# Kernel tuning notes

Measured on AMD Instinct MI355X. Metric: run time of the kernel, lower is better.

The kernel has to match this reference:

```python
import jax, jax.numpy as jnp
import numpy as np

L, B, N, D, H, F = 6, 4, 1024, 1024, 16, 4096
HD = D // H
EPS = 1e-5


def setup_inputs() -> dict:
    key = jax.random.key(0)
    ks = jax.random.split(key, 20)
    s = 0.02
    inp = {
        "feats": jax.random.normal(ks[0], (L, B, N, D), jnp.float32),
        "enc_out": jax.random.normal(ks[1], (B, N, D), jnp.float32),
        "trg_mask": jnp.zeros((1, 1, N, N), jnp.float32),
        "src_mask": jnp.zeros((1, 1, N, N), jnp.float32),
    }
    # stacked per-layer parameters, torch Linear convention W:[out,in]
    names = ["wq1", "wk1", "wv1", "wo1", "wq2", "wk2", "wv2", "wo2"]
    for i, n in enumerate(names):
        inp[n] = jax.random.normal(ks[2 + i], (L, D, D), jnp.float32) * s
        inp["b" + n[1:]] = jnp.zeros((L, D), jnp.float32)
    inp["wf1"] = jax.random.normal(ks[10], (L, F, D), jnp.float32) * s
    inp["bf1"] = jnp.zeros((L, F), jnp.float32)
    inp["wf2"] = jax.random.normal(ks[11], (L, D, F), jnp.float32) * s
    inp["bf2"] = jnp.zeros((L, D), jnp.float32)
    for j in (1, 2, 3):
        inp[f"g{j}"] = jnp.ones((L, D), jnp.float32)
        inp[f"be{j}"] = jnp.zeros((L, D), jnp.float32)
    return inp


def _ln(x, g, b):
    m = jnp.mean(x, -1, keepdims=True)
    v = jnp.mean(jnp.square(x - m), -1, keepdims=True)
    return (x - m) * jax.lax.rsqrt(v + EPS) * g + b


def _heads(x):  # [B,N,D] -> [B,H,N,HD]
    return x.reshape(x.shape[0], x.shape[1], H, HD).transpose(0, 2, 1, 3)


def _mha(q_in, k_in, v_in, Wq, bq, Wk, bk, Wv, bv, Wo, bo, mask):
    q = _heads(q_in @ Wq.T + bq) * (HD ** -0.5)
    k = _heads(k_in @ Wk.T + bk)
    v = _heads(v_in @ Wv.T + bv)
    attn = jnp.einsum("bhid,bhjd->bhij", q, k) + mask
    attn = jax.nn.softmax(attn, axis=-1)
    o = jnp.einsum("bhij,bhjd->bhid", attn, v)
    o = o.transpose(0, 2, 1, 3).reshape(q_in.shape[0], q_in.shape[1], D)
    return o @ Wo.T + bo


def reference(feats, enc_out, trg_mask, src_mask,
              wq1, bq1, wk1, bk1, wv1, bv1, wo1, bo1,
              wq2, bq2, wk2, bk2, wv2, bv2, wo2, bo2,
              wf1, bf1, wf2, bf2, g1, be1, g2, be2, g3, be3):
    x = enc_out
    outs = []
    for l in range(L):
        feat = feats[l]
        dec_out = x
        # cross-attn to encoder output (attn1, src_mask)
        y = _mha(feat, enc_out, enc_out,
                 wq1[l], bq1[l], wk1[l], bk1[l], wv1[l], bv1[l], wo1[l], bo1[l],
                 src_mask) + feat
        y = _ln(y, g1[l], be1[l])
        # attn to previous decoder output (attn2, trg_mask)
        y = _mha(y, dec_out, dec_out,
                 wq2[l], bq2[l], wk2[l], bk2[l], wv2[l], bv2[l], wo2[l], bo2[l],
                 trg_mask) + y
        y = _ln(y, g2[l], be2[l])
        # FFN
        h = jax.nn.relu(y @ wf1[l].T + bf1[l])
        y = _ln(h @ wf2[l].T + bf2[l] + y, g3[l], be3[l])
        outs.append(y)
        x = y
    return jnp.stack(outs)  # [L,B,N,D]
```

## Files before the change

### kernel.cpp

```cpp
#include <hip/hip_runtime.h>
#include <cstdint>
#include <cstddef>

#define Lc 6
#define Bc 4
#define Nc 1024
#define Dc 1024
#define Hn 16
#define HDc 64
#define Fc 4096

static constexpr long BND = (long)Bc * Nc * Dc;
static constexpr long DD  = (long)Dc * Dc;
#define FDl  ((long)Fc * Dc)
static constexpr long BNF = (long)Bc * Nc * Fc;

typedef __attribute__((ext_vector_type(8))) short bf8_t;
typedef __attribute__((ext_vector_type(4))) float f4_t;

__device__ __forceinline__ float b2f(unsigned short u) {
  union { unsigned int i; float f; } v; v.i = ((unsigned int)u) << 16; return v.f;
}
__device__ __forceinline__ unsigned short f2b(float f) {
  union { float f; unsigned int i; } v; v.f = f;
  return (unsigned short)((v.i + 0x7fffu + ((v.i >> 16) & 1u)) >> 16);
}

__device__ __forceinline__ void gl_lds16(const unsigned short* g, unsigned short* l) {
  __builtin_amdgcn_global_load_lds(
      (const __attribute__((address_space(1))) void*)g,
      (__attribute__((address_space(3))) void*)l, 16, 0, 0);
}

__global__ __launch_bounds__(256) void k_cast(const float* __restrict__ x,
                                              unsigned short* __restrict__ y, long n4) {
  long i = (long)blockIdx.x * 256 + threadIdx.x;
  if (i >= n4) return;
  float4 v = ((const float4*)x)[i];
  ushort4 o = { f2b(v.x), f2b(v.y), f2b(v.z), f2b(v.w) };
  ((ushort4*)y)[i] = o;
}

__global__ __launch_bounds__(256) void k_cast2(const float* __restrict__ s1,
                                               const float* __restrict__ s2,
                                               unsigned short* __restrict__ dst) {
  long i4 = (long)blockIdx.x * 256 + threadIdx.x;
  long flat = i4 * 4;
  int l = (int)(flat / (2 * DD));
  long r = flat - (long)l * 2 * DD;
  const float* src = (r < DD) ? (s1 + (long)l * DD + r) : (s2 + (long)l * DD + (r - DD));
  float4 v = *(const float4*)src;
  ushort4 o = { f2b(v.x), f2b(v.y), f2b(v.z), f2b(v.w) };
  *(ushort4*)(dst + flat) = o;
}

__global__ __launch_bounds__(256) void k_bcat2(const float* __restrict__ b1,
                                               const float* __restrict__ b2,
                                               float* __restrict__ dst) {
  int i = blockIdx.x * 256 + threadIdx.x;
  int l = i >> 11, r = i & 2047;
  dst[i] = (r < 1024) ? b1[l * 1024 + r] : b2[l * 1024 + (r - 1024)];
}

__global__ __launch_bounds__(256) void k_packvt2(const unsigned short* __restrict__ KV,
                                                 unsigned short* __restrict__ Vt) {
  __shared__ unsigned short T[64][72];
  const int bh = blockIdx.y, b = bh >> 4, h = bh & 15;
  const int n0 = blockIdx.x * 64;
  const int r = threadIdx.x >> 4;
  const int c4 = (threadIdx.x & 15) * 4;
  const unsigned short* src = KV + ((long)b * Nc + n0) * 2048 + 1024 + h * 64;
  #pragma unroll
  for (int it = 0; it < 4; ++it) {
    ushort4 v = *(const ushort4*)&src[(long)(it * 16 + r) * 2048 + c4];
    *(ushort4*)&T[it * 16 + r][c4] = v;
  }
  __syncthreads();
  unsigned short* dst = Vt + (long)bh * HDc * Nc + n0;
  #pragma unroll
  for (int it = 0; it < 4; ++it) {
    const int d = it * 16 + r;
    ushort4 v = { T[c4 + 0][d], T[c4 + 1][d], T[c4 + 2][d], T[c4 + 3][d] };
    *(ushort4*)&dst[(long)d * Nc + c4] = v;
  }
}

__global__ __launch_bounds__(256) void k_ln(const float* __restrict__ X,
                                            const float* __restrict__ X2,
                                            const float* __restrict__ g,
                                            const float* __restrict__ be,
                                            float* __restrict__ Yf,
                                            unsigned short* __restrict__ Yb) {
  const long row = blockIdx.x;
  const float4* x4 = (const float4*)(X + row * Dc);
  const int tid = threadIdx.x, lane = tid & 63, wave = tid >> 6;
  float4 x = x4[tid];
  if (X2) {
    float4 x2 = ((const float4*)(X2 + row * Dc))[tid];
    x.x += x2.x; x.y += x2.y; x.z += x2.z; x.w += x2.w;
  }
  float s = x.x + x.y + x.z + x.w;
  float q = x.x * x.x + x.y * x.y + x.z * x.z + x.w * x.w;
  #pragma unroll
  for (int o = 32; o > 0; o >>= 1) { s += __shfl_down(s, o); q += __shfl_down(q, o); }
  __shared__ float rs[4], rq[4];
  if (lane == 0) { rs[wave] = s; rq[wave] = q; }
  __syncthreads();
  s = rs[0] + rs[1] + rs[2] + rs[3];
  q = rq[0] + rq[1] + rq[2] + rq[3];
  const float mean = s * (1.f / Dc);
  const float var = q * (1.f / Dc) - mean * mean;
  const float rstd = rsqrtf(var + 1e-5f);
  float4 gv = ((const float4*)g)[tid];
  float4 bv = ((const float4*)be)[tid];
  float4 y;
  y.x = (x.x - mean) * rstd * gv.x + bv.x;
  y.y = (x.y - mean) * rstd * gv.y + bv.y;
  y.z = (x.z - mean) * rstd * gv.z + bv.z;
  y.w = (x.w - mean) * rstd * gv.w + bv.w;
  if (Yf) ((float4*)(Yf + row * Dc))[tid] = y;
  if (Yb) {
    ushort4 o = { f2b(y.x), f2b(y.y), f2b(y.z), f2b(y.w) };
    ((ushort4*)(Yb + row * Dc))[tid] = o;
  }
}

#define QT 64
#define KT 128
#define PRS 132
__global__ __launch_bounds__(256, 2) void k_flash(
    const unsigned short* __restrict__ Q,
    const unsigned short* __restrict__ Kg,
    const unsigned short* __restrict__ Vt,
    const float* __restrict__ mask,
    unsigned short* __restrict__ O, int ldk) {
  __shared__ __align__(16) unsigned short Qs[QT * 64];
  __shared__ __align__(16) unsigned short Ks[KT * 64];
  __shared__ __align__(16) unsigned short Vs[64 * KT];
  __shared__ __align__(16) unsigned short Ps[QT * PRS];

  const int tid = threadIdx.x;
  const int wave = tid >> 6, lane = tid & 63;
  const int lm = lane & 15, quad = lane >> 4;
  const int bh = blockIdx.y;
  const int b = bh >> 4, h = bh & 15;
  const int q0 = blockIdx.x * QT;

  const unsigned short* Qb = Q + ((long)b * Nc + q0) * Dc + h * HDc;
  const unsigned short* Kb = Kg + (long)b * Nc * ldk + h * HDc;
  const unsigned short* Vb = Vt + (long)bh * HDc * Nc;

  const int sr = tid >> 3, sc = (tid & 7) * 8;
  #pragma unroll
  for (int it = 0; it < QT / 32; ++it)
    gl_lds16(Qb + (long)(it * 32 + sr) * Dc + sc, &Qs[(it * 32 + sr) * 64 + sc]);

  f4_t Oa[4];
  #pragma unroll
  for (int jh = 0; jh < 4; ++jh) Oa[jh] = {0.f, 0.f, 0.f, 0.f};
  float m_run[4], l_run[4];
  #pragma unroll
  for (int r = 0; r < 4; ++r) { m_run[r] = -1e30f; l_run[r] = 0.f; }

  const int row_q = wave * 16 + quad * 4;
  const int vr = tid >> 4, vc = (tid & 15) * 8;

  for (int t = 0; t < Nc / KT; ++t) {
    #pragma unroll
    for (int it = 0; it < KT / 32; ++it)
      gl_lds16(Kb + (long)(t * KT + it * 32 + sr) * ldk + sc, &Ks[(it * 32 + sr) * 64 + sc]);
    #pragma unroll
    for (int it = 0; it < 4; ++it)
      gl_lds16(Vb + (long)(it * 16 + vr) * Nc + t * KT + vc, &Vs[(it * 16 + vr) * KT + vc]);
    __syncthreads();

    f4_t Sa[8];
    #pragma unroll
    for (int j = 0; j < 8; ++j) Sa[j] = {0.f, 0.f, 0.f, 0.f};
    #pragma unroll
    for (int kk = 0; kk < 2; ++kk) {
      const int kq = kk * 32 + quad * 8;
      bf8_t aq = *(const bf8_t*)&Qs[(wave * 16 + lm) * 64 + kq];
      #pragma unroll
      for (int j = 0; j < 8; ++j) {
        bf8_t bk = *(const bf8_t*)&Ks[(j * 16 + lm) * 64 + kq];
        Sa[j] = __builtin_amdgcn_mfma_f32_16x16x32_bf16(aq, bk, Sa[j], 0, 0, 0);
      }
    }

    float p[8][4], alpha[4];
    #pragma unroll
    for (int r = 0; r < 4; ++r) {
      const float* mrow = mask + (long)(q0 + row_q + r) * Nc + t * KT + lm;
      float sv[8];
      float mt = -1e30f;
      #pragma unroll
      for (int j = 0; j < 8; ++j) { sv[j] = Sa[j][r] + mrow[j * 16]; mt = fmaxf(mt, sv[j]); }
      #pragma unroll
      for (int o = 1; o < 16; o <<= 1) mt = fmaxf(mt, __shfl_xor(mt, o));
      const float mn = fmaxf(m_run[r], mt);
      alpha[r] = __expf(m_run[r] - mn);
      m_run[r] = mn;
      float sp = 0.f;
      #pragma unroll
      for (int j = 0; j < 8; ++j) { float e = __expf(sv[j] - mn); p[j][r] = e; sp += e; }
      #pragma unroll
      for (int o = 1; o < 16; o <<= 1) sp += __shfl_xor(sp, o);
      l_run[r] = l_run[r] * alpha[r] + sp;
    }

    #pragma unroll
    for (int r = 0; r < 4; ++r)
      #pragma unroll
      for (int j = 0; j < 8; ++j)
        Ps[(row_q + r) * PRS + j * 16 + lm] = f2b(p[j][r]);
    __syncthreads();

    #pragma unroll
    for (int jh = 0; jh < 4; ++jh)
      #pragma unroll
      for (int r = 0; r < 4; ++r) Oa[jh][r] *= alpha[r];
    #pragma unroll
    for (int kk = 0; kk < 4; ++kk) {
      const int kp = kk * 32 + quad * 8;
      bf8_t ap = *(const bf8_t*)&Ps[(wave * 16 + lm) * PRS + kp];
      #pragma unroll
      for (int jh = 0; jh < 4; ++jh) {
        bf8_t bv = *(const bf8_t*)&Vs[(jh * 16 + lm) * KT + kp];
        Oa[jh] = __builtin_amdgcn_mfma_f32_16x16x32_bf16(ap, bv, Oa[jh], 0, 0, 0);
      }
    }
    __syncthreads();
  }

  #pragma unroll
  for (int r = 0; r < 4; ++r) {
    const float inv = 1.f / l_run[r];
    unsigned short* orow = O + ((long)b * Nc + q0 + row_q + r) * Dc + h * HDc;
    #pragma unroll
    for (int jh = 0; jh < 4; ++jh) orow[jh * 16 + lm] = f2b(Oa[jh][r] * inv);
  }
}

template <int BM, int BN, int MW, int NW>
__device__ __forceinline__ void mfma_loop(
    const unsigned short* __restrict__ A, const unsigned short* __restrict__ W,
    int K, int lda, int ldb, int m0, int n0,
    unsigned short* As, unsigned short* Bs,
    f4_t (&acc)[BM / MW / 16][BN / NW / 16]) {
  constexpr int WM = BM / MW, WN = BN / NW;
  constexpr int FM = WM / 16, FN = WN / 16;
  const int tid = threadIdx.x;
  const int wave = tid >> 6, lane = tid & 63;
  const int wm = wave / NW, wn = wave % NW;
  const int sr = tid >> 3, sc = (tid & 7) * 8;
  const int lm = lane & 15, quad = lane >> 4;

  for (int k0 = 0; k0 < K; k0 += 64) {
    #pragma unroll
    for (int it = 0; it < BM / 32; ++it) {
      const int rr = it * 32 + sr;
      gl_lds16(A + (long)(m0 + rr) * lda + (k0 + sc), &As[rr * 64 + sc]);
    }
    #pragma unroll
    for (int it = 0; it < BN / 32; ++it) {
      const int rr = it * 32 + sr;
      gl_lds16(W + (long)(n0 + rr) * ldb + (k0 + sc), &Bs[rr * 64 + sc]);
    }
    __syncthreads();
    #pragma unroll
    for (int kk = 0; kk < 2; ++kk) {
      const int kq = kk * 32 + quad * 8;
      bf8_t af[FM], bfr[FN];
      #pragma unroll
      for (int i = 0; i < FM; ++i)
        af[i] = *(const bf8_t*)&As[(wm * WM + i * 16 + lm) * 64 + kq];
      #pragma unroll
      for (int j = 0; j < FN; ++j)
        bfr[j] = *(const bf8_t*)&Bs[(wn * WN + j * 16 + lm) * 64 + kq];
      #pragma unroll
      for (int i = 0; i < FM; ++i)
        #pragma unroll
        for (int j = 0; j < FN; ++j)
          acc[i][j] = __builtin_amdgcn_mfma_f32_16x16x32_bf16(af[i], bfr[j], acc[i][j], 0, 0, 0);
    }
    __syncthreads();
  }
}

template <int BM, int BN, int MW, int NW>
__global__ __launch_bounds__(256, 2) void gemm_bt(
    const unsigned short* __restrict__ A, const unsigned short* __restrict__ W,
    const float* __restrict__ bias, const float* __restrict__ res,
    float* __restrict__ Cf, unsigned short* __restrict__ Cb,
    int K, int lda, int ldb, int ldc, float scale, int relu) {
  constexpr int WM = BM / MW, WN = BN / NW;
  constexpr int FM = WM / 16, FN = WN / 16;

  __shared__ __align__(16) unsigned short As[BM * 64];
  __shared__ __align__(16) unsigned short Bs[BN * 64];

  const int tid = threadIdx.x;
  const int wave = tid >> 6, lane = tid & 63;
  const int wm = wave / NW, wn = wave % NW;
  const int n0 = blockIdx.x * BN, m0 = blockIdx.y * BM;
  const int lm = lane & 15, quad = lane >> 4;

  f4_t acc[FM][FN];
  const f4_t zero = {0.f, 0.f, 0.f, 0.f};
  #pragma unroll
  for (int i = 0; i < FM; ++i)
    #pragma unroll
    for (int j = 0; j < FN; ++j) acc[i][j] = zero;

  mfma_loop<BM, BN, MW, NW>(A, W, K, lda, ldb, m0, n0, As, Bs, acc);

  #pragma unroll
  for (int i = 0; i < FM; ++i) {
    const int grow_base = m0 + wm * WM + i * 16 + quad * 4;
    #pragma unroll
    for (int j = 0; j < FN; ++j) {
      const int gcol = n0 + wn * WN + j * 16 + lm;
      const float bi = bias ? bias[gcol] : 0.f;
      #pragma unroll
      for (int r = 0; r < 4; ++r) {
        float v = (acc[i][j][r] + bi) * scale;
        if (relu) v = fmaxf(v, 0.f);
        const long cidx = (long)(grow_base + r) * ldc + gcol;
        if (res) v += res[cidx];
        if (Cf) Cf[cidx] = v;
        if (Cb) Cb[cidx] = f2b(v);
      }
    }
  }
}

__global__ __launch_bounds__(256, 2) void gemm_qkv(
    const unsigned short* __restrict__ Aq,  const unsigned short* __restrict__ Wq,
    const float* __restrict__ bq,
    const unsigned short* __restrict__ Ak1, const unsigned short* __restrict__ Wkv1,
    const float* __restrict__ bkv1,
    const unsigned short* __restrict__ Ak2, const unsigned short* __restrict__ Wkv2,
    const float* __restrict__ bkv2,
    unsigned short* __restrict__ Cq, unsigned short* __restrict__ Ckv1,
    unsigned short* __restrict__ Ckv2) {
  __shared__ __align__(16) unsigned short As[128 * 64];
  __shared__ __align__(16) unsigned short Bs[128 * 64];

  const int bx = blockIdx.x;
  const unsigned short *A, *W;
  const float* bias;
  unsigned short* C;
  int ldc, n0;
  float scale;
  if (bx < 8)       { A = Aq;  W = Wq;   bias = bq;   C = Cq;   ldc = 1024; n0 = bx * 128;        scale = 0.125f; }
  else if (bx < 24) { A = Ak1; W = Wkv1; bias = bkv1; C = Ckv1; ldc = 2048; n0 = (bx - 8) * 128;  scale = 1.f; }
  else              { A = Ak2; W = Wkv2; bias = bkv2; C = Ckv2; ldc = 2048; n0 = (bx - 24) * 128; scale = 1.f; }
  const int m0 = blockIdx.y * 128;

  const int tid = threadIdx.x;
  const int wave = tid >> 6, lane = tid & 63;
  const int wm = wave / 2, wn = wave % 2;
  const int lm = lane & 15, quad = lane >> 4;

  f4_t acc[4][4];
  const f4_t zero = {0.f, 0.f, 0.f, 0.f};
  #pragma unroll
  for (int i = 0; i < 4; ++i)
    #pragma unroll
    for (int j = 0; j < 4; ++j) acc[i][j] = zero;

  mfma_loop<128, 128, 2, 2>(A, W, 1024, 1024, 1024, m0, n0, As, Bs, acc);

  #pragma unroll
  for (int i = 0; i < 4; ++i) {
    const int grow_base = m0 + wm * 64 + i * 16 + quad * 4;
    #pragma unroll
    for (int j = 0; j < 4; ++j) {
      const int gcol = n0 + wn * 64 + j * 16 + lm;
      const float bi = bias[gcol];
      #pragma unroll
      for (int r = 0; r < 4; ++r) {
        float v = (acc[i][j][r] + bi) * scale;
        C[(long)(grow_base + r) * ldc + gcol] = f2b(v);
      }
    }
  }
}

__global__ __launch_bounds__(256, 2) void gemm_f2s(
    const unsigned short* __restrict__ A, const unsigned short* __restrict__ W,
    const float* __restrict__ bias, const float* __restrict__ res,
    float* __restrict__ P0, float* __restrict__ P1) {
  __shared__ __align__(16) unsigned short As[128 * 64];
  __shared__ __align__(16) unsigned short Bs[128 * 64];

  const int z = blockIdx.z;
  const int kbeg = z * 2048;
  const int n0 = blockIdx.x * 128, m0 = blockIdx.y * 128;

  const int tid = threadIdx.x;
  const int wave = tid >> 6, lane = tid & 63;
  const int wm = wave / 2, wn = wave % 2;
  const int lm = lane & 15, quad = lane >> 4;

  f4_t acc[4][4];
  const f4_t zero = {0.f, 0.f, 0.f, 0.f};
  #pragma unroll
  for (int i = 0; i < 4; ++i)
    #pragma unroll
    for (int j = 0; j < 4; ++j) acc[i][j] = zero;

  mfma_loop<128, 128, 2, 2>(A + kbeg, W + kbeg, 2048, 4096, 4096, m0, n0, As, Bs, acc);

  float* P = z ? P1 : P0;
  #pragma unroll
  for (int i = 0; i < 4; ++i) {
    const int grow_base = m0 + wm * 64 + i * 16 + quad * 4;
    #pragma unroll
    for (int j = 0; j < 4; ++j) {
      const int gcol = n0 + wn * 64 + j * 16 + lm;
      const float bi = bias[gcol];
      #pragma unroll
      for (int r = 0; r < 4; ++r) {
        const long cidx = (long)(grow_base + r) * Dc + gcol;
        float v = acc[i][j][r];
        if (z == 0) v += bi + res[cidx];
        P[cidx] = v;
      }
    }
  }
}

extern "C" void kernel_launch(void* const* d_in, const int* in_sizes, int n_in,
                              void* d_out, int out_size, void* d_ws, size_t ws_size,
                              hipStream_t stream) {
  const float* feats    = (const float*)d_in[0];
  const float* enc      = (const float*)d_in[1];
  const float* trg_mask = (const float*)d_in[2];
  const float* src_mask = (const float*)d_in[3];
  const float* wq1 = (const float*)d_in[4];  const float* bq1 = (const float*)d_in[5];
  const float* wk1 = (const float*)d_in[6];  const float* bk1 = (const float*)d_in[7];
  const float* wv1 = (const float*)d_in[8];  const float* bv1 = (const float*)d_in[9];
  const float* wo1 = (const float*)d_in[10]; const float* bo1 = (const float*)d_in[11];
  const float* wq2 = (const float*)d_in[12]; const float* bq2 = (const float*)d_in[13];
  const float* wk2 = (const float*)d_in[14]; const float* bk2 = (const float*)d_in[15];
  const float* wv2 = (const float*)d_in[16]; const float* bv2 = (const float*)d_in[17];
  const float* wo2 = (const float*)d_in[18]; const float* bo2 = (const float*)d_in[19];
  const float* wf1 = (const float*)d_in[20]; const float* bf1 = (const float*)d_in[21];
  const float* wf2 = (const float*)d_in[22]; const float* bf2 = (const float*)d_in[23];
  const float* g1  = (const float*)d_in[24]; const float* be1 = (const float*)d_in[25];
  const float* g2  = (const float*)d_in[26]; const float* be2 = (const float*)d_in[27];
  const float* g3  = (const float*)d_in[28]; const float* be3 = (const float*)d_in[29];
  float* out = (float*)d_out;

  char* wsp = (char*)d_ws;
  size_t off = 0;
  auto alloc = [&](size_t bytes) -> void* {
    void* p = wsp + off;
    off = (off + bytes + 255) & ~(size_t)255;
    return p;
  };
  unsigned short* wq1b  = (unsigned short*)alloc(Lc * DD * 2);
  unsigned short* wo1b  = (unsigned short*)alloc(Lc * DD * 2);
  unsigned short* wq2b  = (unsigned short*)alloc(Lc * DD * 2);
  unsigned short* wo2b  = (unsigned short*)alloc(Lc * DD * 2);
  unsigned short* wkv1b = (unsigned short*)alloc(Lc * 2 * DD * 2);
  unsigned short* wkv2b = (unsigned short*)alloc(Lc * 2 * DD * 2);
  unsigned short* wf1b  = (unsigned short*)alloc(Lc * FDl * 2);
  unsigned short* wf2b  = (unsigned short*)alloc(Lc * FDl * 2);
  float* bkv1c = (float*)alloc(Lc * 2048 * 4);
  float* bkv2c = (float*)alloc(Lc * 2048 * 4);
  unsigned short* encb    = (unsigned short*)alloc(BND * 2);
  unsigned short* featall = (unsigned short*)alloc(Lc * BND * 2);
  unsigned short* xb    = (unsigned short*)alloc(BND * 2);
  unsigned short* y1b   = (unsigned short*)alloc(BND * 2);
  unsigned short* y2b   = (unsigned short*)alloc(BND * 2);
  unsigned short* qb    = (unsigned short*)alloc(BND * 2);
  unsigned short* kvb   = (unsigned short*)alloc((long)Bc * Nc * 2048 * 2);
  unsigned short* kvb2  = (unsigned short*)alloc((long)Bc * Nc * 2048 * 2);
  unsigned short* vtb   = (unsigned short*)alloc(BND * 2);
  unsigned short* vtb2  = (unsigned short*)alloc(BND * 2);
  unsigned short* ob    = (unsigned short*)alloc(BND * 2);
  unsigned short* hb    = (unsigned short*)alloc(BNF * 2);
  float* y1f  = (float*)alloc(BND * 4);
  float* y2f  = (float*)alloc(BND * 4);
  float* pre  = (float*)alloc(BND * 4);
  float* pre2 = (float*)alloc(BND * 4);
  (void)ws_size; (void)in_sizes; (void)n_in; (void)out_size;

  auto cast = [&](const float* src, unsigned short* dst, long n) {
    long n4 = n / 4;
    k_cast<<<dim3((unsigned)((n4 + 255) / 256)), dim3(256), 0, stream>>>(src, dst, n4);
  };
  auto cast2 = [&](const float* s1, const float* s2, unsigned short* dst) {
    k_cast2<<<dim3((unsigned)(Lc * 2 * DD / 4 / 256)), dim3(256), 0, stream>>>(s1, s2, dst);
  };
  auto bcat2 = [&](const float* b1, const float* b2, float* dst) {
    k_bcat2<<<dim3(Lc * 2048 / 256), dim3(256), 0, stream>>>(b1, b2, dst);
  };
  auto gemm128 = [&](const unsigned short* A, const unsigned short* Wp, const float* bias,
                     const float* res, float* Cf, unsigned short* Cb,
                     int M, int Nout, int K, int lda, int ldb, int ldc, float scale, int relu) {
    gemm_bt<128, 128, 2, 2><<<dim3(Nout / 128, M / 128), dim3(256), 0, stream>>>(
        A, Wp, bias, res, Cf, Cb, K, lda, ldb, ldc, scale, relu);
  };
  auto gemm64 = [&](const unsigned short* A, const unsigned short* Wp, const float* bias,
                    const float* res, float* Cf, unsigned short* Cb,
                    int M, int Nout, int K, int lda, int ldb, int ldc, float scale, int relu) {
    gemm_bt<128, 64, 2, 2><<<dim3(Nout / 64, M / 128), dim3(256), 0, stream>>>(
        A, Wp, bias, res, Cf, Cb, K, lda, ldb, ldc, scale, relu);
  };
  auto flash = [&](const unsigned short* Kg, const unsigned short* Vt, const float* mask) {
    k_flash<<<dim3(Nc / QT, Bc * Hn), dim3(256), 0, stream>>>(qb, Kg, Vt, mask, ob, 2048);
  };
  auto ln = [&](const float* X, const float* X2, const float* gg, const float* bb,
                float* Yf, unsigned short* Yb) {
    k_ln<<<dim3(Bc * Nc), dim3(256), 0, stream>>>(X, X2, gg, bb, Yf, Yb);
  };
  auto packvt = [&](const unsigned short* kv, unsigned short* vt) {
    k_packvt2<<<dim3(Nc / 64, Bc * Hn), dim3(256), 0, stream>>>(kv, vt);
  };

  cast(wq1, wq1b, Lc * DD); cast(wo1, wo1b, Lc * DD);
  cast(wq2, wq2b, Lc * DD); cast(wo2, wo2b, Lc * DD);
  cast2(wk1, wv1, wkv1b);   cast2(wk2, wv2, wkv2b);
  bcat2(bk1, bv1, bkv1c);   bcat2(bk2, bv2, bkv2c);
  cast(wf1, wf1b, Lc * FDl); cast(wf2, wf2b, Lc * FDl);
  cast(enc, encb, BND);
  cast(feats, featall, (long)Lc * BND);

  for (int l = 0; l < Lc; ++l) {
    const float* featl = feats + (long)l * BND;
    const unsigned short* featb = featall + (long)l * BND;
    const unsigned short* kv2src = (l == 0) ? encb : xb;

    gemm_qkv<<<dim3(40, 32), dim3(256), 0, stream>>>(
        featb, wq1b + (long)l * DD, bq1 + l * Dc,
        encb,  wkv1b + (long)l * 2 * DD, bkv1c + l * 2048,
        kv2src, wkv2b + (long)l * 2 * DD, bkv2c + l * 2048,
        qb, kvb, kvb2);
    packvt(kvb, vtb);
    packvt(kvb2, vtb2);

    flash(kvb, vtb, src_mask);
    gemm64(ob, wo1b + (long)l * DD, bo1 + l * Dc, featl, pre, nullptr,
           Bc * Nc, Dc, Dc, Dc, Dc, Dc, 1.f, 0);
    ln(pre, nullptr, g1 + l * Dc, be1 + l * Dc, y1f, y1b);

    gemm64(y1b, wq2b + (long)l * DD, bq2 + l * Dc, nullptr, nullptr, qb,
           Bc * Nc, Dc, Dc, Dc, Dc, Dc, 0.125f, 0);
    flash(kvb2, vtb2, trg_mask);
    gemm64(ob, wo2b + (long)l * DD, bo2 + l * Dc, y1f, pre, nullptr,
           Bc * Nc, Dc, Dc, Dc, Dc, Dc, 1.f, 0);
    ln(pre, nullptr, g2 + l * Dc, be2 + l * Dc, y2f, y2b);

    gemm128(y2b, wf1b + (long)l * FDl, bf1 + l * Fc, nullptr, nullptr, hb,
            Bc * Nc, Fc, Dc, Dc, Dc, Fc, 1.f, 1);
    gemm_f2s<<<dim3(8, 32, 2), dim3(256), 0, stream>>>(
        hb, wf2b + (long)l * FDl, bf2 + l * Dc, y2f, pre, pre2);
    ln(pre, pre2, g3 + l * Dc, be3 + l * Dc, out + (long)l * BND, xb);
  }
}
```

Measured before the change: 3.541 ms.

## Swizzle flash-attention LDS layout, remap workgroups, use bf16 masks, fuse V transposes

Applies an XOR swizzle to the Q/K/V tiles in LDS of the flash kernel to reduce bank conflicts on MFMA operand reads. It remaps the workgroup index so that blocks sharing the same batch-head are grouped per XCD, and raises wave priority around the MFMA sections. The masks are pre-cast to bf16 to halve the bandwidth spent reading them, and the two V-transpose launches are merged into one. Casting the masks to bf16 loses precision for arbitrary non-zero mask values.

```diff
diff --git a/kernel.cpp b/kernel.cpp
--- a/kernel.cpp
+++ b/kernel.cpp
@@ -14,6 +14,7 @@
 static constexpr long DD  = (long)Dc * Dc;
 #define FDl  ((long)Fc * Dc)
 static constexpr long BNF = (long)Bc * Nc * Fc;
+static constexpr long NN  = (long)Nc * Nc;
 
 typedef __attribute__((ext_vector_type(8))) short bf8_t;
 typedef __attribute__((ext_vector_type(4))) float f4_t;
@@ -62,10 +63,15 @@
   dst[i] = (r < 1024) ? b1[l * 1024 + r] : b2[l * 1024 + (r - 1024)];
 }
 
-__global__ __launch_bounds__(256) void k_packvt2(const unsigned short* __restrict__ KV,
-                                                 unsigned short* __restrict__ Vt) {
+__global__ __launch_bounds__(256) void k_packvt2(const unsigned short* __restrict__ KV1,
+                                                 unsigned short* __restrict__ Vt1,
+                                                 const unsigned short* __restrict__ KV2,
+                                                 unsigned short* __restrict__ Vt2) {
   __shared__ unsigned short T[64][72];
-  const int bh = blockIdx.y, b = bh >> 4, h = bh & 15;
+  const int yy = blockIdx.y;
+  const unsigned short* KV = (yy < 64) ? KV1 : KV2;
+  unsigned short* Vt = (yy < 64) ? Vt1 : Vt2;
+  const int bh = yy & 63, b = bh >> 4, h = bh & 15;
   const int n0 = blockIdx.x * 64;
   const int r = threadIdx.x >> 4;
   const int c4 = (threadIdx.x & 15) * 4;
@@ -132,7 +138,7 @@
     const unsigned short* __restrict__ Q,
     const unsigned short* __restrict__ Kg,
     const unsigned short* __restrict__ Vt,
-    const float* __restrict__ mask,
+    const unsigned short* __restrict__ mask,
     unsigned short* __restrict__ O, int ldk) {
   __shared__ __align__(16) unsigned short Qs[QT * 64];
   __shared__ __align__(16) unsigned short Ks[KT * 64];
@@ -142,18 +148,22 @@
   const int tid = threadIdx.x;
   const int wave = tid >> 6, lane = tid & 63;
   const int lm = lane & 15, quad = lane >> 4;
-  const int bh = blockIdx.y;
+
+  const int wg = blockIdx.y * gridDim.x + blockIdx.x;
+  const int wid = (wg & 7) * 128 + (wg >> 3);
+  const int bh = wid >> 4;
   const int b = bh >> 4, h = bh & 15;
-  const int q0 = blockIdx.x * QT;
+  const int q0 = (wid & 15) * QT;
 
   const unsigned short* Qb = Q + ((long)b * Nc + q0) * Dc + h * HDc;
   const unsigned short* Kb = Kg + (long)b * Nc * ldk + h * HDc;
   const unsigned short* Vb = Vt + (long)bh * HDc * Nc;
 
   const int sr = tid >> 3, sc = (tid & 7) * 8;
+  const int scs = sc ^ ((sr & 7) << 3);
   #pragma unroll
   for (int it = 0; it < QT / 32; ++it)
-    gl_lds16(Qb + (long)(it * 32 + sr) * Dc + sc, &Qs[(it * 32 + sr) * 64 + sc]);
+    gl_lds16(Qb + (long)(it * 32 + sr) * Dc + scs, &Qs[(it * 32 + sr) * 64 + sc]);
 
   f4_t Oa[4];
   #pragma unroll
@@ -164,38 +174,42 @@
 
   const int row_q = wave * 16 + quad * 4;
   const int vr = tid >> 4, vc = (tid & 15) * 8;
+  const int vcs = vc ^ ((vr & 7) << 3);
+  const int sw = (lm & 7) << 3;
 
   for (int t = 0; t < Nc / KT; ++t) {
     #pragma unroll
     for (int it = 0; it < KT / 32; ++it)
-      gl_lds16(Kb + (long)(t * KT + it * 32 + sr) * ldk + sc, &Ks[(it * 32 + sr) * 64 + sc]);
+      gl_lds16(Kb + (long)(t * KT + it * 32 + sr) * ldk + scs, &Ks[(it * 32 + sr) * 64 + sc]);
     #pragma unroll
     for (int it = 0; it < 4; ++it)
-      gl_lds16(Vb + (long)(it * 16 + vr) * Nc + t * KT + vc, &Vs[(it * 16 + vr) * KT + vc]);
+      gl_lds16(Vb + (long)(it * 16 + vr) * Nc + t * KT + (vcs), &Vs[(it * 16 + vr) * KT + vc]);
     __syncthreads();
 
     f4_t Sa[8];
     #pragma unroll
     for (int j = 0; j < 8; ++j) Sa[j] = {0.f, 0.f, 0.f, 0.f};
+    __builtin_amdgcn_s_setprio(1);
     #pragma unroll
     for (int kk = 0; kk < 2; ++kk) {
       const int kq = kk * 32 + quad * 8;
-      bf8_t aq = *(const bf8_t*)&Qs[(wave * 16 + lm) * 64 + kq];
+      bf8_t aq = *(const bf8_t*)&Qs[(wave * 16 + lm) * 64 + (kq ^ sw)];
       #pragma unroll
       for (int j = 0; j < 8; ++j) {
-        bf8_t bk = *(const bf8_t*)&Ks[(j * 16 + lm) * 64 + kq];
+        bf8_t bk = *(const bf8_t*)&Ks[(j * 16 + lm) * 64 + (kq ^ sw)];
         Sa[j] = __builtin_amdgcn_mfma_f32_16x16x32_bf16(aq, bk, Sa[j], 0, 0, 0);
       }
     }
+    __builtin_amdgcn_s_setprio(0);
 
     float p[8][4], alpha[4];
     #pragma unroll
     for (int r = 0; r < 4; ++r) {
-      const float* mrow = mask + (long)(q0 + row_q + r) * Nc + t * KT + lm;
+      const unsigned short* mrow = mask + (long)(q0 + row_q + r) * Nc + t * KT + lm;
       float sv[8];
       float mt = -1e30f;
       #pragma unroll
-      for (int j = 0; j < 8; ++j) { sv[j] = Sa[j][r] + mrow[j * 16]; mt = fmaxf(mt, sv[j]); }
+      for (int j = 0; j < 8; ++j) { sv[j] = Sa[j][r] + b2f(mrow[j * 16]); mt = fmaxf(mt, sv[j]); }
       #pragma unroll
       for (int o = 1; o < 16; o <<= 1) mt = fmaxf(mt, __shfl_xor(mt, o));
       const float mn = fmaxf(m_run[r], mt);
@@ -220,16 +234,18 @@
     for (int jh = 0; jh < 4; ++jh)
       #pragma unroll
       for (int r = 0; r < 4; ++r) Oa[jh][r] *= alpha[r];
+    __builtin_amdgcn_s_setprio(1);
     #pragma unroll
     for (int kk = 0; kk < 4; ++kk) {
       const int kp = kk * 32 + quad * 8;
       bf8_t ap = *(const bf8_t*)&Ps[(wave * 16 + lm) * PRS + kp];
       #pragma unroll
       for (int jh = 0; jh < 4; ++jh) {
-        bf8_t bv = *(const bf8_t*)&Vs[(jh * 16 + lm) * KT + kp];
+        bf8_t bv = *(const bf8_t*)&Vs[(jh * 16 + lm) * KT + (kp ^ sw)];
         Oa[jh] = __builtin_amdgcn_mfma_f32_16x16x32_bf16(ap, bv, Oa[jh], 0, 0, 0);
       }
     }
+    __builtin_amdgcn_s_setprio(0);
     __syncthreads();
   }
 
@@ -473,6 +489,8 @@
   float* bkv2c = (float*)alloc(Lc * 2048 * 4);
   unsigned short* encb    = (unsigned short*)alloc(BND * 2);
   unsigned short* featall = (unsigned short*)alloc(Lc * BND * 2);
+  unsigned short* smaskb  = (unsigned short*)alloc(NN * 2);
+  unsigned short* tmaskb  = (unsigned short*)alloc(NN * 2);
   unsigned short* xb    = (unsigned short*)alloc(BND * 2);
   unsigned short* y1b   = (unsigned short*)alloc(BND * 2);
   unsigned short* y2b   = (unsigned short*)alloc(BND * 2);
@@ -511,15 +529,15 @@
     gemm_bt<128, 64, 2, 2><<<dim3(Nout / 64, M / 128), dim3(256), 0, stream>>>(
         A, Wp, bias, res, Cf, Cb, K, lda, ldb, ldc, scale, relu);
   };
-  auto flash = [&](const unsigned short* Kg, const unsigned short* Vt, const float* mask) {
+  auto flash = [&](const unsigned short* Kg, const unsigned short* Vt, const unsigned short* mask) {
     k_flash<<<dim3(Nc / QT, Bc * Hn), dim3(256), 0, stream>>>(qb, Kg, Vt, mask, ob, 2048);
   };
   auto ln = [&](const float* X, const float* X2, const float* gg, const float* bb,
                 float* Yf, unsigned short* Yb) {
     k_ln<<<dim3(Bc * Nc), dim3(256), 0, stream>>>(X, X2, gg, bb, Yf, Yb);
   };
-  auto packvt = [&](const unsigned short* kv, unsigned short* vt) {
-    k_packvt2<<<dim3(Nc / 64, Bc * Hn), dim3(256), 0, stream>>>(kv, vt);
+  auto packvt_dual = [&]() {
+    k_packvt2<<<dim3(Nc / 64, 2 * Bc * Hn), dim3(256), 0, stream>>>(kvb, vtb, kvb2, vtb2);
   };
 
   cast(wq1, wq1b, Lc * DD); cast(wo1, wo1b, Lc * DD);
@@ -529,6 +547,8 @@
   cast(wf1, wf1b, Lc * FDl); cast(wf2, wf2b, Lc * FDl);
   cast(enc, encb, BND);
   cast(feats, featall, (long)Lc * BND);
+  cast(src_mask, smaskb, NN);
+  cast(trg_mask, tmaskb, NN);
 
   for (int l = 0; l < Lc; ++l) {
     const float* featl = feats + (long)l * BND;
@@ -540,17 +560,16 @@
         encb,  wkv1b + (long)l * 2 * DD, bkv1c + l * 2048,
         kv2src, wkv2b + (long)l * 2 * DD, bkv2c + l * 2048,
         qb, kvb, kvb2);
-    packvt(kvb, vtb);
-    packvt(kvb2, vtb2);
-
-    flash(kvb, vtb, src_mask);
+    packvt_dual();
+
+    flash(kvb, vtb, smaskb);
     gemm64(ob, wo1b + (long)l * DD, bo1 + l * Dc, featl, pre, nullptr,
            Bc * Nc, Dc, Dc, Dc, Dc, Dc, 1.f, 0);
     ln(pre, nullptr, g1 + l * Dc, be1 + l * Dc, y1f, y1b);
 
     gemm64(y1b, wq2b + (long)l * DD, bq2 + l * Dc, nullptr, nullptr, qb,
            Bc * Nc, Dc, Dc, Dc, Dc, Dc, 0.125f, 0);
-    flash(kvb2, vtb2, trg_mask);
+    flash(kvb2, vtb2, tmaskb);
     gemm64(ob, wo2b + (long)l * DD, bo2 + l * Dc, y1f, pre, nullptr,
            Bc * Nc, Dc, Dc, Dc, Dc, Dc, 1.f, 0);
     ln(pre, nullptr, g2 + l * Dc, be2 + l * Dc, y2f, y2b);
```

Measured after the change: 3.163 ms. 1.12x faster.
